# Kernel tuning notes

Measured on AMD Instinct MI355X. Metric: run time of the kernel, lower is better.

## Reference

```python
import jax, jax.numpy as jnp
import numpy as np

B_, L_, D_, N_ = 4, 4096, 1024, 32


def setup_inputs() -> dict:
    key = jax.random.key(0)
    ks = jax.random.split(key, 8)
    def n(k, shape, s=0.02):
        return jax.random.normal(k, shape, jnp.float32) * s
    return {
        "x": jax.random.normal(ks[0], (B_, L_, D_), jnp.float32),
        "in_w": n(ks[1], (2 * D_, D_)),
        "in_b": jnp.zeros((2 * D_,), jnp.float32),
        "conv_w": n(ks[2], (D_, 1, 4), 0.1),
        "conv_b": jnp.zeros((D_,), jnp.float32),
        "A_log": -2.0 + 0.1 * jax.random.normal(ks[3], (D_, N_), jnp.float32),
        "B_w": n(ks[4], (N_, D_)),
        "B_b": jnp.zeros((N_,), jnp.float32),
        "C_w": n(ks[5], (N_, D_)),
        "C_b": jnp.zeros((N_,), jnp.float32),
        "out_w": n(ks[6], (D_, D_)),
        "out_b": jnp.zeros((D_,), jnp.float32),
        "ln_w": jnp.ones((D_,), jnp.float32),
        "ln_b": jnp.zeros((D_,), jnp.float32),
    }


def reference(x, in_w, in_b, conv_w, conv_b, A_log, B_w, B_b, C_w, C_b, out_w, out_b, ln_w, ln_b):
    Bsz, L, D = x.shape
    residual = x
    # in_proj and chunk
    xz = x @ in_w.T + in_b                       # (B, L, 2D)
    xa, z = xz[..., :D], xz[..., D:]
    # depthwise conv1d, kernel=4, padding=2 -> length L+1 (matches torch)
    xc = jax.lax.conv_general_dilated(
        xa.transpose(0, 2, 1), conv_w, (1,), [(2, 2)],
        feature_group_count=D, dimension_numbers=("NCH", "OIH", "NCH"))
    xc = xc + conv_b[None, :, None]
    xc = jax.nn.silu(xc.transpose(0, 2, 1))      # (B, L+1, D)
    A = -jnp.exp(jnp.clip(A_log, -5.0, 2.0))     # (D, N)
    Bm = xc @ B_w.T + B_b                        # (B, L+1, N)
    Cm = xc @ C_w.T + C_b                        # (B, L+1, N)
    # only first L steps are used by the loop
    xs = (xc[:, :L].transpose(1, 0, 2),          # (L, B, D)
          Bm[:, :L].transpose(1, 0, 2),          # (L, B, N)
          Cm[:, :L].transpose(1, 0, 2))          # (L, B, N)
    s0 = jnp.zeros((Bsz, D, A.shape[1]), x.dtype)

    def step(s, t):
        x_t, b_t, c_t = t
        s = jnp.clip(s * A + b_t[:, None, :] * x_t[:, :, None], -10.0, 10.0)
        y = jnp.sum(c_t[:, None, :] * s, axis=-1)  # (B, D)
        return s, y

    _, ys = jax.lax.scan(step, s0, xs)           # ys: (L, B, D)
    y = ys.transpose(1, 0, 2) * jax.nn.silu(z)   # (B, L, D)
    out = y @ out_w.T + out_b
    h = out + residual
    mu = jnp.mean(h, axis=-1, keepdims=True)
    var = jnp.var(h, axis=-1, keepdims=True)
    return (h - mu) / jnp.sqrt(var + 1e-5) * ln_w + ln_b
```

## Files before the change

kernel.cpp:

```cpp
#include <hip/hip_runtime.h>
#include <hip/hip_bf16.h>

#define B_ 4
#define L_ 4096
#define D_ 1024
#define N_ 32
#define MTOT (B_*L_)
#define TCH 32
#define WARM 6
#define STEPS (TCH + WARM)
#define SROWS 48

typedef __bf16 bf16;
typedef __attribute__((ext_vector_type(8))) __bf16 bf16x8;
typedef __attribute__((ext_vector_type(4))) __bf16 bf16x4;
typedef __attribute__((ext_vector_type(4))) float f32x4;
typedef __attribute__((ext_vector_type(2))) float f32x2;

__device__ __forceinline__ void gload_lds16(const void* gsrc, void* ldst) {
  __builtin_amdgcn_global_load_lds(
      (__attribute__((address_space(1))) void*)(unsigned long long)gsrc,
      (__attribute__((address_space(3))) void*)ldst, 16, 0, 0);
}

__global__ __launch_bounds__(256) void cvt_w_kernel(
    const float* __restrict__ in_w, const float* __restrict__ out_w,
    const float* __restrict__ B_w, const float* __restrict__ C_w,
    const float* __restrict__ A_log, const float* __restrict__ B_b,
    const float* __restrict__ C_b, const float* __restrict__ x,
    bf16* __restrict__ in_wb, bf16* __restrict__ out_wb, bf16* __restrict__ bcw,
    float* __restrict__ Aexp, float* __restrict__ bias_bc,
    bf16* __restrict__ xb) {
  const int stride = gridDim.x * 256;
  const int i0 = blockIdx.x * 256 + threadIdx.x;
  for (int j = i0; j < (B_ * L_ * D_) / 4; j += stride) {
    const float4 v = ((const float4*)x)[j];
    bf16x4 o = {(bf16)v.x, (bf16)v.y, (bf16)v.z, (bf16)v.w};
    ((bf16x4*)xb)[j] = o;
  }
  for (int j = i0; j < 2 * D_ * D_; j += stride) in_wb[j] = (bf16)in_w[j];
  for (int j = i0; j < D_ * D_; j += stride) out_wb[j] = (bf16)out_w[j];
  for (int j = i0; j < N_ * D_; j += stride) {
    bcw[j] = (bf16)B_w[j];
    bcw[N_ * D_ + j] = (bf16)C_w[j];
  }
  for (int j = i0; j < D_ * N_; j += stride)
    Aexp[j] = -expf(fminf(fmaxf(A_log[j], -5.f), 2.f));
  if (i0 < N_) { bias_bc[i0] = B_b[i0]; bias_bc[N_ + i0] = C_b[i0]; }
}

template <bool OUT_BF16, bool ADD_RESID>
__global__ __launch_bounds__(256) void gemm8_kernel(
    const bf16* __restrict__ Ag, const bf16* __restrict__ Wg,
    const float* __restrict__ bias, const float* __restrict__ resid,
    void* __restrict__ Cg, int Ncols, int K, int nbm, int nbn) {
  constexpr int BK = 64;
  __shared__ bf16 As[2][128][64];
  __shared__ bf16 Bs[2][128][64];
  const int tid = threadIdx.x;
  const int lane = tid & 63;
  const int wid = tid >> 6;
  const int wm = wid >> 1, wn = wid & 1;
  const int l15 = lane & 15, lh = lane >> 4, r7 = l15 & 7;

  const int sx = nbm >> 3;
  const int xcd = blockIdx.x & 7;
  const int pos = blockIdx.x >> 3;
  const int bx = xcd * sx + pos / nbn;
  const int by = pos % nbn;
  const int row0 = bx * 128, col0 = by * 128;
  const int nt = K / BK;

  const bf16* aSrc[4]; const bf16* bSrc[4]; int dstOff[4];
#pragma unroll
  for (int j = 0; j < 4; ++j) {
    const int c = tid + j * 256;
    const int row = c >> 3, lcol = c & 7;
    const int gcol = lcol ^ (row & 7);
    aSrc[j] = Ag + (size_t)(row0 + row) * K + gcol * 8;
    bSrc[j] = Wg + (size_t)(col0 + row) * K + gcol * 8;
    dstOff[j] = c * 8;
  }

  f32x4 acc[4][4] = {};

#pragma unroll
  for (int j = 0; j < 4; ++j) gload_lds16(aSrc[j], &As[0][0][0] + dstOff[j]);
#pragma unroll
  for (int j = 0; j < 4; ++j) gload_lds16(bSrc[j], &Bs[0][0][0] + dstOff[j]);
#pragma unroll
  for (int j = 0; j < 4; ++j) gload_lds16(aSrc[j] + BK, &As[1][0][0] + dstOff[j]);
#pragma unroll
  for (int j = 0; j < 4; ++j) gload_lds16(bSrc[j] + BK, &Bs[1][0][0] + dstOff[j]);
  asm volatile("s_waitcnt vmcnt(8)" ::: "memory");
  __builtin_amdgcn_sched_barrier(0);
  __builtin_amdgcn_s_barrier();
  __builtin_amdgcn_sched_barrier(0);

  for (int t = 0; t < nt; ++t) {
    const int p = t & 1;
    const bf16* Ab = &As[p][0][0];
    const bf16* Bb = &Bs[p][0][0];
    bf16x8 af[4][2], bfr[4][2];
#pragma unroll
    for (int mi = 0; mi < 4; ++mi)
#pragma unroll
      for (int kk = 0; kk < 2; ++kk)
        af[mi][kk] = *(const bf16x8*)(Ab + (wm * 64 + mi * 16 + l15) * 64 +
                                      (((kk * 4 + lh) ^ r7) * 8));
#pragma unroll
    for (int ni = 0; ni < 4; ++ni)
#pragma unroll
      for (int kk = 0; kk < 2; ++kk)
        bfr[ni][kk] = *(const bf16x8*)(Bb + (wn * 64 + ni * 16 + l15) * 64 +
                                       (((kk * 4 + lh) ^ r7) * 8));
    asm volatile("s_waitcnt lgkmcnt(0)" ::: "memory");
    __builtin_amdgcn_sched_barrier(0);
    __builtin_amdgcn_s_barrier();
    __builtin_amdgcn_sched_barrier(0);
    if (t + 2 < nt) {
      const int k2 = (t + 2) * BK;
#pragma unroll
      for (int j = 0; j < 4; ++j) gload_lds16(aSrc[j] + k2, &As[p][0][0] + dstOff[j]);
#pragma unroll
      for (int j = 0; j < 4; ++j) gload_lds16(bSrc[j] + k2, &Bs[p][0][0] + dstOff[j]);
    }
    __builtin_amdgcn_s_setprio(1);
#pragma unroll
    for (int kk = 0; kk < 2; ++kk)
#pragma unroll
      for (int mi = 0; mi < 4; ++mi)
#pragma unroll
        for (int ni = 0; ni < 4; ++ni)
          acc[mi][ni] = __builtin_amdgcn_mfma_f32_16x16x32_bf16(
              af[mi][kk], bfr[ni][kk], acc[mi][ni], 0, 0, 0);
    __builtin_amdgcn_s_setprio(0);
    if (t + 2 < nt) asm volatile("s_waitcnt vmcnt(8)" ::: "memory");
    else            asm volatile("s_waitcnt vmcnt(0)" ::: "memory");
    __builtin_amdgcn_sched_barrier(0);
    __builtin_amdgcn_s_barrier();
    __builtin_amdgcn_sched_barrier(0);
  }

#pragma unroll
  for (int mi = 0; mi < 4; ++mi) {
#pragma unroll
    for (int ni = 0; ni < 4; ++ni) {
      const int c = col0 + wn * 64 + ni * 16 + l15;
      const float bv = bias[c];
#pragma unroll
      for (int j = 0; j < 4; ++j) {
        const int r = row0 + wm * 64 + mi * 16 + lh * 4 + j;
        float v = acc[mi][ni][j] + bv;
        if constexpr (ADD_RESID) v += resid[(size_t)r * Ncols + c];
        if constexpr (OUT_BF16)
          ((bf16*)Cg)[(size_t)r * Ncols + c] = (bf16)v;
        else
          ((float*)Cg)[(size_t)r * Ncols + c] = v;
      }
    }
  }
}

template <int BM, int BN, int WAVES_M, int WAVES_N, bool OUT_BF16, bool ADD_RESID>
__global__ __launch_bounds__(256) void gemm_kernel(
    const bf16* __restrict__ Ag, const bf16* __restrict__ Wg,
    const float* __restrict__ bias, const float* __restrict__ resid,
    void* __restrict__ Cg, int Ncols, int K) {
  constexpr int BK = 32;
  constexpr int WM = BM / WAVES_M;
  constexpr int WN = BN / WAVES_N;
  constexpr int MI = WM / 16;
  constexpr int NI = WN / 16;
  __shared__ alignas(16) bf16 As[BM][BK];
  __shared__ alignas(16) bf16 Bs[BN][BK];
  const int tid = threadIdx.x;
  const int lane = tid & 63;
  const int wid = tid >> 6;
  const int wm = wid / WAVES_N;
  const int wn = wid % WAVES_N;
  const int l15 = lane & 15;
  const int lh = lane >> 4;
  const int row0 = blockIdx.x * BM;
  const int col0 = blockIdx.y * BN;

  f32x4 acc[MI][NI] = {};

  for (int k0 = 0; k0 < K; k0 += BK) {
#pragma unroll
    for (int i = 0; i < (BM * BK * 2 / 16) / 256; ++i) {
      const int chunk = tid + i * 256;
      const int o = chunk * 16;
      const int r = o >> 6;
      const int kb = (o & 63) >> 1;
      gload_lds16(Ag + (size_t)(row0 + r) * K + (k0 + kb),
                  (bf16*)&As[0][0] + (size_t)(wid * 64 + i * 256) * 8);
    }
#pragma unroll
    for (int i = 0; i < (BN * BK * 2 / 16) / 256; ++i) {
      const int chunk = tid + i * 256;
      const int o = chunk * 16;
      const int r = o >> 6;
      const int kb = (o & 63) >> 1;
      gload_lds16(Wg + (size_t)(col0 + r) * K + (k0 + kb),
                  (bf16*)&Bs[0][0] + (size_t)(wid * 64 + i * 256) * 8);
    }
    __syncthreads();

    bf16x8 af[MI], bfv[NI];
#pragma unroll
    for (int mi = 0; mi < MI; ++mi)
      af[mi] = *(const bf16x8*)&As[wm * WM + mi * 16 + l15][lh * 8];
#pragma unroll
    for (int ni = 0; ni < NI; ++ni)
      bfv[ni] = *(const bf16x8*)&Bs[wn * WN + ni * 16 + l15][lh * 8];
#pragma unroll
    for (int mi = 0; mi < MI; ++mi)
#pragma unroll
      for (int ni = 0; ni < NI; ++ni)
        acc[mi][ni] = __builtin_amdgcn_mfma_f32_16x16x32_bf16(
            af[mi], bfv[ni], acc[mi][ni], 0, 0, 0);
    __syncthreads();
  }

#pragma unroll
  for (int mi = 0; mi < MI; ++mi) {
#pragma unroll
    for (int ni = 0; ni < NI; ++ni) {
      const int c = col0 + wn * WN + ni * 16 + l15;
      const float bv = bias[c];
#pragma unroll
      for (int j = 0; j < 4; ++j) {
        const int r = row0 + wm * WM + mi * 16 + lh * 4 + j;
        float v = acc[mi][ni][j] + bv;
        if constexpr (ADD_RESID) v += resid[(size_t)r * Ncols + c];
        if constexpr (OUT_BF16)
          ((bf16*)Cg)[(size_t)r * Ncols + c] = (bf16)v;
        else
          ((float*)Cg)[(size_t)r * Ncols + c] = v;
      }
    }
  }
}

__global__ __launch_bounds__(256) void conv_silu_kernel(
    const bf16* __restrict__ xz, const float* __restrict__ conv_w,
    const float* __restrict__ conv_b, bf16* __restrict__ xc) {
  const int idx = blockIdx.x * 256 + threadIdx.x;
  const int d8 = idx & (D_ / 8 - 1);
  const int bt = idx >> 7;
  const int t = bt & (L_ - 1);
  const int b = bt >> 12;
  const int d = d8 * 8;

  float accv[8];
  float4 w4[8];
#pragma unroll
  for (int j = 0; j < 8; ++j) {
    accv[j] = conv_b[d + j];
    w4[j] = *(const float4*)(conv_w + (size_t)(d + j) * 4);
  }
#pragma unroll
  for (int k = 0; k < 4; ++k) {
    const int tt = t + k - 2;
    if (tt < 0 || tt >= L_) continue;
    const bf16x8 xv = *(const bf16x8*)(xz + (size_t)(b * L_ + tt) * (2 * D_) + d);
#pragma unroll
    for (int j = 0; j < 8; ++j) {
      const float wk = (k == 0) ? w4[j].x : (k == 1) ? w4[j].y : (k == 2) ? w4[j].z : w4[j].w;
      accv[j] += (float)xv[j] * wk;
    }
  }
  bf16x8 o;
#pragma unroll
  for (int j = 0; j < 8; ++j) {
    const float v = accv[j];
    o[j] = (bf16)(v / (1.f + __expf(-v)));
  }
  *(bf16x8*)(xc + (size_t)(b * L_ + t) * D_ + d) = o;
}

#define SCAN_STEP(PB, PC, XT)                                             \
  {                                                                       \
    const f32x2 xt2 = {XT, XT};                                           \
    yac = (f32x2){0.f, 0.f};                                              \
    _Pragma("unroll")                                                     \
    for (int q = 0; q < 8; ++q) {                                         \
      f32x2 v = __builtin_elementwise_fma(s[q], Ar[q], PB[q] * xt2);      \
      s[q] = v;                                                           \
      yac = __builtin_elementwise_fma(PC[q], v, yac);                     \
    }                                                                     \
  }

__device__ __forceinline__ void load8v(f32x2* dst, const float* p) {
#pragma unroll
  for (int q = 0; q < 4; ++q) {
    const f32x4 v = ((const f32x4*)p)[q];
    dst[2 * q]     = (f32x2){v.x, v.y};
    dst[2 * q + 1] = (f32x2){v.z, v.w};
  }
}

__global__ __launch_bounds__(256)
__attribute__((amdgpu_waves_per_eu(4)))
void scan_kernel(
    const bf16* __restrict__ xc, const float* __restrict__ BC,
    const bf16* __restrict__ xz, const float* __restrict__ Aexp,
    bf16* __restrict__ y) {
  const int dg = blockIdx.x, chunk = blockIdx.y, b = blockIdx.z;
  const int tid = threadIdx.x;
  const int wid = tid >> 6;
  const int nh = tid & 1;
  const int dl = tid >> 1;
  const int d = dg * 128 + dl;
  const int t0 = chunk * TCH;
  const int warm = (t0 >= WARM) ? WARM : 0;
  const int tstart = t0 - warm;

  __shared__ float bcs[SROWS][64];
  __shared__ bf16 xcs[SROWS][128];
  __shared__ bf16 zs[TCH][128];

#pragma unroll
  for (int i = 0; i < 3; ++i)
    gload_lds16(BC + ((size_t)b * L_ + tstart) * 64 + (size_t)(tid + i * 256) * 4,
                (float*)&bcs[0][0] + (size_t)(wid * 64 + i * 256) * 4);
#pragma unroll
  for (int i = 0; i < 3; ++i) {
    const int c = tid + i * 256;
    gload_lds16(xc + ((size_t)b * L_ + tstart + (c >> 4)) * D_ + dg * 128 + (c & 15) * 8,
                (bf16*)&xcs[0][0] + (size_t)(wid * 64 + i * 256) * 8);
  }
#pragma unroll
  for (int i = 0; i < 2; ++i) {
    const int c = tid + i * 256;
    gload_lds16(xz + ((size_t)b * L_ + t0 + (c >> 4)) * (2 * D_) + D_ + dg * 128 + (c & 15) * 8,
                (bf16*)&zs[0][0] + (size_t)(wid * 64 + i * 256) * 8);
  }

  f32x2 Ar[8], s[8];
  {
    const f32x2* ap = (const f32x2*)(Aexp + (size_t)d * N_ + nh * 16);
#pragma unroll
    for (int q = 0; q < 8; ++q) { Ar[q] = ap[q]; s[q] = (f32x2){0.f, 0.f}; }
  }

  bf16* yp = y + (size_t)b * L_ * D_ + d;
  f32x2 yac;

  __syncthreads();

  for (int i = 0; i < warm; ++i) {
    const float xt = (float)xcs[i][dl];
    const f32x2 xt2 = {xt, xt};
    const f32x2* rb = (const f32x2*)&bcs[i][nh * 16];
#pragma unroll
    for (int q = 0; q < 8; ++q)
      s[q] = __builtin_elementwise_fma(s[q], Ar[q], rb[q] * xt2);
  }

  f32x2 pbA[8], pcA[8], pbB[8], pcB[8];
  float pxA, pzA, pxB, pzB;
  load8v(pbA, &bcs[warm][nh * 16]);
  load8v(pcA, &bcs[warm][32 + nh * 16]);
  pxA = (float)xcs[warm][dl];
  pzA = (float)zs[0][dl];

  for (int j = 0; j < TCH; j += 2) {
    load8v(pbB, &bcs[warm + j + 1][nh * 16]);
    load8v(pcB, &bcs[warm + j + 1][32 + nh * 16]);
    pxB = (float)xcs[warm + j + 1][dl];
    pzB = (float)zs[j + 1][dl];
    SCAN_STEP(pbA, pcA, pxA);
    {
      float yacc = yac.x + yac.y;
      yacc += __shfl_xor(yacc, 1);
      if (nh == 0) {
        const float sz = pzA / (1.f + __expf(-pzA));
        yp[(size_t)(t0 + j) * D_] = (bf16)(yacc * sz);
      }
    }
    load8v(pbA, &bcs[warm + j + 2][nh * 16]);
    load8v(pcA, &bcs[warm + j + 2][32 + nh * 16]);
    pxA = (float)xcs[warm + j + 2][dl];
    pzA = (float)zs[(j + 2 < TCH) ? (j + 2) : 0][dl];
    SCAN_STEP(pbB, pcB, pxB);
    {
      float yacc = yac.x + yac.y;
      yacc += __shfl_xor(yacc, 1);
      if (nh == 0) {
        const float sz = pzB / (1.f + __expf(-pzB));
        yp[(size_t)(t0 + j + 1) * D_] = (bf16)(yacc * sz);
      }
    }
  }
}

__global__ __launch_bounds__(256) void ln2_kernel(const bf16* __restrict__ g,
                                                  const float* __restrict__ x,
                                                  const float* __restrict__ ln_w,
                                                  const float* __restrict__ ln_b,
                                                  float* __restrict__ out) {
  const int row = blockIdx.x;
  const int tid = threadIdx.x;
  const bf16x4 gv = ((const bf16x4*)(g + (size_t)row * D_))[tid];
  const float4 xv = ((const float4*)(x + (size_t)row * D_))[tid];
  float4 v;
  v.x = (float)gv[0] + xv.x;
  v.y = (float)gv[1] + xv.y;
  v.z = (float)gv[2] + xv.z;
  v.w = (float)gv[3] + xv.w;
  float sum = v.x + v.y + v.z + v.w;
  float sq = v.x * v.x + v.y * v.y + v.z * v.z + v.w * v.w;
#pragma unroll
  for (int off = 32; off >= 1; off >>= 1) {
    sum += __shfl_xor(sum, off);
    sq += __shfl_xor(sq, off);
  }
  __shared__ float red[8];
  const int wid = tid >> 6;
  if ((tid & 63) == 0) { red[wid] = sum; red[4 + wid] = sq; }
  __syncthreads();
  sum = red[0] + red[1] + red[2] + red[3];
  sq = red[4] + red[5] + red[6] + red[7];
  const float mu = sum * (1.f / D_);
  const float var = sq * (1.f / D_) - mu * mu;
  const float inv = rsqrtf(var + 1e-5f);
  const float4 w4 = ((const float4*)ln_w)[tid];
  const float4 b4 = ((const float4*)ln_b)[tid];
  float4 o;
  o.x = (v.x - mu) * inv * w4.x + b4.x;
  o.y = (v.y - mu) * inv * w4.y + b4.y;
  o.z = (v.z - mu) * inv * w4.z + b4.z;
  o.w = (v.w - mu) * inv * w4.w + b4.w;
  ((float4*)(out + (size_t)row * D_))[tid] = o;
}

extern "C" void kernel_launch(void* const* d_in, const int* in_sizes, int n_in,
                              void* d_out, int out_size, void* d_ws, size_t ws_size,
                              hipStream_t stream) {
  (void)in_sizes; (void)n_in; (void)out_size; (void)ws_size;
  const float* x      = (const float*)d_in[0];
  const float* in_w   = (const float*)d_in[1];
  const float* in_b   = (const float*)d_in[2];
  const float* conv_w = (const float*)d_in[3];
  const float* conv_b = (const float*)d_in[4];
  const float* A_log  = (const float*)d_in[5];
  const float* B_w    = (const float*)d_in[6];
  const float* B_b    = (const float*)d_in[7];
  const float* C_w    = (const float*)d_in[8];
  const float* C_b    = (const float*)d_in[9];
  const float* out_w  = (const float*)d_in[10];
  const float* out_b  = (const float*)d_in[11];
  const float* ln_w   = (const float*)d_in[12];
  const float* ln_b   = (const float*)d_in[13];
  float* out = (float*)d_out;

  char* ws = (char*)d_ws;
  bf16* xb_y    = (bf16*)(ws + 0);
  bf16* xz      = (bf16*)(ws + 33554432);
  bf16* xc_g    = (bf16*)(ws + 100663296);
  float* BC     = (float*)(ws + 134217728);
  bf16* in_wb   = (bf16*)(ws + 138412032);
  bf16* out_wb  = (bf16*)(ws + 142606336);
  bf16* bcw     = (bf16*)(ws + 144703488);
  float* Aexp   = (float*)(ws + 144834560);
  float* bias_bc= (float*)(ws + 144965632);

  cvt_w_kernel<<<2048, 256, 0, stream>>>(in_w, out_w, B_w, C_w, A_log, B_b, C_b,
                                         x, in_wb, out_wb, bcw, Aexp, bias_bc, xb_y);
  gemm8_kernel<true, false>
      <<<128 * 16, 256, 0, stream>>>(xb_y, in_wb, in_b, nullptr, xz, 2 * D_, D_, 128, 16);
  conv_silu_kernel<<<(B_ * L_ * D_ / 8) / 256, 256, 0, stream>>>(xz, conv_w, conv_b, xc_g);
  gemm_kernel<64, 64, 2, 2, false, false>
      <<<dim3(MTOT / 64, 1), 256, 0, stream>>>(xc_g, bcw, bias_bc, nullptr, BC, 64, D_);
  scan_kernel<<<dim3(D_ / 128, L_ / TCH, B_), 256, 0, stream>>>(xc_g, BC, xz, Aexp, xb_y);
  gemm8_kernel<true, false>
      <<<128 * 8, 256, 0, stream>>>(xb_y, out_wb, out_b, nullptr, xc_g, D_, D_, 128, 8);
  ln2_kernel<<<MTOT, 256, 0, stream>>>(xc_g, x, ln_w, ln_b, out);
}
```

Measured before the change: 297.8 us.

## Replace 128x128 GEMM with 256x256-tile 8-wave kernel with interleaved staging

Replaces the 128x128-tile, 4-wave bf16 GEMM used for the in_proj and out_proj matmuls with a 256x256-tile, 512-thread kernel. Each wave computes a 128x64 sub-tile in four quarter phases, and global-to-LDS loads for the next K-steps are interleaved between the MFMA phases. Larger tiles raise arithmetic intensity and cut global traffic per FLOP. In exchange, the grid shrinks to 512 and 256 blocks, which can leave CUs underfilled on the out_proj launch, and the extra barriers per K-step add sync cost.

New measurement: 295.2 us. No clear change (-0.9%).

```diff
diff --git a/kernel.cpp b/kernel.cpp
--- a/kernel.cpp
+++ b/kernel.cpp
@@ -22,6 +22,11 @@
       (__attribute__((address_space(1))) void*)(unsigned long long)gsrc,
       (__attribute__((address_space(3))) void*)ldst, 16, 0, 0);
 }
+
+#define BARR  do { __builtin_amdgcn_s_barrier(); \
+                   __builtin_amdgcn_sched_barrier(0); } while (0)
+#define LGKM0 do { asm volatile("s_waitcnt lgkmcnt(0)" ::: "memory"); \
+                   __builtin_amdgcn_sched_barrier(0); } while (0)
 
 __global__ __launch_bounds__(256) void cvt_w_kernel(
     const float* __restrict__ in_w, const float* __restrict__ out_w,
@@ -49,114 +54,162 @@
   if (i0 < N_) { bias_bc[i0] = B_b[i0]; bias_bc[N_ + i0] = C_b[i0]; }
 }
 
-template <bool OUT_BF16, bool ADD_RESID>
-__global__ __launch_bounds__(256) void gemm8_kernel(
+__global__ __launch_bounds__(512, 1) void gemm256_kernel(
     const bf16* __restrict__ Ag, const bf16* __restrict__ Wg,
-    const float* __restrict__ bias, const float* __restrict__ resid,
-    void* __restrict__ Cg, int Ncols, int K, int nbm, int nbn) {
-  constexpr int BK = 64;
-  __shared__ bf16 As[2][128][64];
-  __shared__ bf16 Bs[2][128][64];
+    const float* __restrict__ bias, bf16* __restrict__ Cg,
+    int Ncols, int K, int nbm, int nbn) {
+  __shared__ bf16 lds[8][128][64];
   const int tid = threadIdx.x;
   const int lane = tid & 63;
   const int wid = tid >> 6;
-  const int wm = wid >> 1, wn = wid & 1;
-  const int l15 = lane & 15, lh = lane >> 4, r7 = l15 & 7;
+  const int wm = wid >> 2;
+  const int wn = wid & 3;
+  const int l15 = lane & 15, lh = lane >> 4;
 
   const int sx = nbm >> 3;
   const int xcd = blockIdx.x & 7;
   const int pos = blockIdx.x >> 3;
   const int bx = xcd * sx + pos / nbn;
   const int by = pos % nbn;
-  const int row0 = bx * 128, col0 = by * 128;
-  const int nt = K / BK;
-
-  const bf16* aSrc[4]; const bf16* bSrc[4]; int dstOff[4];
-#pragma unroll
-  for (int j = 0; j < 4; ++j) {
-    const int c = tid + j * 256;
-    const int row = c >> 3, lcol = c & 7;
-    const int gcol = lcol ^ (row & 7);
-    aSrc[j] = Ag + (size_t)(row0 + row) * K + gcol * 8;
-    bSrc[j] = Wg + (size_t)(col0 + row) * K + gcol * 8;
-    dstOff[j] = c * 8;
-  }
-
-  f32x4 acc[4][4] = {};
-
-#pragma unroll
-  for (int j = 0; j < 4; ++j) gload_lds16(aSrc[j], &As[0][0][0] + dstOff[j]);
-#pragma unroll
-  for (int j = 0; j < 4; ++j) gload_lds16(bSrc[j], &Bs[0][0][0] + dstOff[j]);
-#pragma unroll
-  for (int j = 0; j < 4; ++j) gload_lds16(aSrc[j] + BK, &As[1][0][0] + dstOff[j]);
-#pragma unroll
-  for (int j = 0; j < 4; ++j) gload_lds16(bSrc[j] + BK, &Bs[1][0][0] + dstOff[j]);
-  asm volatile("s_waitcnt vmcnt(8)" ::: "memory");
+  const int row0 = bx * 256, col0 = by * 256;
+  const int nt = K / 64;
+
+  const bf16* aS0; const bf16* aS1; const bf16* bS0; const bf16* bS1;
+  int dO0, dO1;
+  {
+    const int c0 = tid, c1 = tid + 512;
+    const int r0 = c0 >> 3, r1 = c1 >> 3;
+    const int g0 = (c0 & 7) ^ (r0 & 7), g1 = (c1 & 7) ^ (r1 & 7);
+    aS0 = Ag + (size_t)(row0 + r0) * K + g0 * 8;
+    aS1 = Ag + (size_t)(row0 + r1) * K + g1 * 8;
+    bS0 = Wg + (size_t)(col0 + r0) * K + g0 * 8;
+    bS1 = Wg + (size_t)(col0 + r1) * K + g1 * 8;
+    dO0 = c0 * 8; dO1 = c1 * 8;
+  }
+
+#define STAGE_A(T, HALF) do {                                               \
+    const size_t off_ = (size_t)(HALF) * 128 * K + (size_t)(T) * 64;        \
+    bf16* dst_ = &lds[((T) & 1) * 4 + (HALF)][0][0];                        \
+    gload_lds16(aS0 + off_, dst_ + dO0);                                    \
+    gload_lds16(aS1 + off_, dst_ + dO1); } while (0)
+#define STAGE_B(T, HALF) do {                                               \
+    const size_t off_ = (size_t)(HALF) * 128 * K + (size_t)(T) * 64;        \
+    bf16* dst_ = &lds[((T) & 1) * 4 + 2 + (HALF)][0][0];                    \
+    gload_lds16(bS0 + off_, dst_ + dO0);                                    \
+    gload_lds16(bS1 + off_, dst_ + dO1); } while (0)
+
+  f32x4 acc[8][4] = {};
+
+  STAGE_A(0, 0); STAGE_A(0, 1); STAGE_B(0, 0); STAGE_B(0, 1);
+  STAGE_B(1, 0); STAGE_B(1, 1);
+  asm volatile("s_waitcnt vmcnt(4)" ::: "memory");
   __builtin_amdgcn_sched_barrier(0);
-  __builtin_amdgcn_s_barrier();
-  __builtin_amdgcn_sched_barrier(0);
-
-  for (int t = 0; t < nt; ++t) {
-    const int p = t & 1;
-    const bf16* Ab = &As[p][0][0];
-    const bf16* Bb = &Bs[p][0][0];
-    bf16x8 af[4][2], bfr[4][2];
-#pragma unroll
-    for (int mi = 0; mi < 4; ++mi)
-#pragma unroll
-      for (int kk = 0; kk < 2; ++kk)
-        af[mi][kk] = *(const bf16x8*)(Ab + (wm * 64 + mi * 16 + l15) * 64 +
-                                      (((kk * 4 + lh) ^ r7) * 8));
-#pragma unroll
-    for (int ni = 0; ni < 4; ++ni)
-#pragma unroll
-      for (int kk = 0; kk < 2; ++kk)
-        bfr[ni][kk] = *(const bf16x8*)(Bb + (wn * 64 + ni * 16 + l15) * 64 +
-                                       (((kk * 4 + lh) ^ r7) * 8));
-    asm volatile("s_waitcnt lgkmcnt(0)" ::: "memory");
+  BARR;
+
+  for (int T = 0; T < nt; ++T) {
+    const int p = T & 1;
+    const bf16* Aseg = &lds[p * 4 + wm][0][0];
+    const bf16* Bseg = &lds[p * 4 + 2 + (wn >> 1)][0][0];
+    const int brow0 = (wn & 1) * 64;
+    bf16x8 af[4][2], bfv[4][2];
+    const bool s1 = (T + 1 < nt), s2 = (T + 2 < nt);
+
+    if (s1) STAGE_A(T + 1, 0);
+#pragma unroll
+    for (int mi = 0; mi < 4; ++mi) {
+      const int r = mi * 16 + l15, sw = r & 7;
+      af[mi][0] = *(const bf16x8*)(Aseg + r * 64 + ((lh ^ sw)) * 8);
+      af[mi][1] = *(const bf16x8*)(Aseg + r * 64 + (((4 + lh) ^ sw)) * 8);
+    }
+#pragma unroll
+    for (int ni = 0; ni < 2; ++ni) {
+      const int r = brow0 + ni * 16 + l15, sw = r & 7;
+      bfv[ni][0] = *(const bf16x8*)(Bseg + r * 64 + ((lh ^ sw)) * 8);
+      bfv[ni][1] = *(const bf16x8*)(Bseg + r * 64 + (((4 + lh) ^ sw)) * 8);
+    }
+    BARR; LGKM0;
+    __builtin_amdgcn_s_setprio(1);
+#pragma unroll
+    for (int kk = 0; kk < 2; ++kk)
+#pragma unroll
+      for (int mi = 0; mi < 4; ++mi)
+#pragma unroll
+        for (int ni = 0; ni < 2; ++ni)
+          acc[mi][ni] = __builtin_amdgcn_mfma_f32_16x16x32_bf16(
+              af[mi][kk], bfv[ni][kk], acc[mi][ni], 0, 0, 0);
+    __builtin_amdgcn_s_setprio(0);
+    BARR;
+
+    if (s1) STAGE_A(T + 1, 1);
+#pragma unroll
+    for (int ni = 2; ni < 4; ++ni) {
+      const int r = brow0 + ni * 16 + l15, sw = r & 7;
+      bfv[ni][0] = *(const bf16x8*)(Bseg + r * 64 + ((lh ^ sw)) * 8);
+      bfv[ni][1] = *(const bf16x8*)(Bseg + r * 64 + (((4 + lh) ^ sw)) * 8);
+    }
+    BARR; LGKM0;
+    __builtin_amdgcn_s_setprio(1);
+#pragma unroll
+    for (int kk = 0; kk < 2; ++kk)
+#pragma unroll
+      for (int mi = 0; mi < 4; ++mi)
+#pragma unroll
+        for (int ni = 2; ni < 4; ++ni)
+          acc[mi][ni] = __builtin_amdgcn_mfma_f32_16x16x32_bf16(
+              af[mi][kk], bfv[ni][kk], acc[mi][ni], 0, 0, 0);
+    __builtin_amdgcn_s_setprio(0);
+    BARR;
+
+    if (s2) STAGE_B(T + 2, 0);
+#pragma unroll
+    for (int mi = 0; mi < 4; ++mi) {
+      const int r = (mi + 4) * 16 + l15, sw = r & 7;
+      af[mi][0] = *(const bf16x8*)(Aseg + r * 64 + ((lh ^ sw)) * 8);
+      af[mi][1] = *(const bf16x8*)(Aseg + r * 64 + (((4 + lh) ^ sw)) * 8);
+    }
+    BARR; LGKM0;
+    __builtin_amdgcn_s_setprio(1);
+#pragma unroll
+    for (int kk = 0; kk < 2; ++kk)
+#pragma unroll
+      for (int mi = 0; mi < 4; ++mi)
+#pragma unroll
+        for (int ni = 0; ni < 2; ++ni)
+          acc[mi + 4][ni] = __builtin_amdgcn_mfma_f32_16x16x32_bf16(
+              af[mi][kk], bfv[ni][kk], acc[mi + 4][ni], 0, 0, 0);
+    __builtin_amdgcn_s_setprio(0);
+    BARR;
+
+    if (s2) STAGE_B(T + 2, 1);
+    BARR;
+    __builtin_amdgcn_s_setprio(1);
+#pragma unroll
+    for (int kk = 0; kk < 2; ++kk)
+#pragma unroll
+      for (int mi = 0; mi < 4; ++mi)
+#pragma unroll
+        for (int ni = 2; ni < 4; ++ni)
+          acc[mi + 4][ni] = __builtin_amdgcn_mfma_f32_16x16x32_bf16(
+              af[mi][kk], bfv[ni][kk], acc[mi + 4][ni], 0, 0, 0);
+    __builtin_amdgcn_s_setprio(0);
+    if (s2) asm volatile("s_waitcnt vmcnt(4)" ::: "memory");
+    else    asm volatile("s_waitcnt vmcnt(0)" ::: "memory");
     __builtin_amdgcn_sched_barrier(0);
-    __builtin_amdgcn_s_barrier();
-    __builtin_amdgcn_sched_barrier(0);
-    if (t + 2 < nt) {
-      const int k2 = (t + 2) * BK;
-#pragma unroll
-      for (int j = 0; j < 4; ++j) gload_lds16(aSrc[j] + k2, &As[p][0][0] + dstOff[j]);
-#pragma unroll
-      for (int j = 0; j < 4; ++j) gload_lds16(bSrc[j] + k2, &Bs[p][0][0] + dstOff[j]);
-    }
-    __builtin_amdgcn_s_setprio(1);
-#pragma unroll
-    for (int kk = 0; kk < 2; ++kk)
-#pragma unroll
-      for (int mi = 0; mi < 4; ++mi)
-#pragma unroll
-        for (int ni = 0; ni < 4; ++ni)
-          acc[mi][ni] = __builtin_amdgcn_mfma_f32_16x16x32_bf16(
-              af[mi][kk], bfr[ni][kk], acc[mi][ni], 0, 0, 0);
-    __builtin_amdgcn_s_setprio(0);
-    if (t + 2 < nt) asm volatile("s_waitcnt vmcnt(8)" ::: "memory");
-    else            asm volatile("s_waitcnt vmcnt(0)" ::: "memory");
-    __builtin_amdgcn_sched_barrier(0);
-    __builtin_amdgcn_s_barrier();
-    __builtin_amdgcn_sched_barrier(0);
-  }
-
-#pragma unroll
-  for (int mi = 0; mi < 4; ++mi) {
+    BARR;
+  }
+#undef STAGE_A
+#undef STAGE_B
+
+#pragma unroll
+  for (int mi = 0; mi < 8; ++mi) {
 #pragma unroll
     for (int ni = 0; ni < 4; ++ni) {
       const int c = col0 + wn * 64 + ni * 16 + l15;
       const float bv = bias[c];
 #pragma unroll
       for (int j = 0; j < 4; ++j) {
-        const int r = row0 + wm * 64 + mi * 16 + lh * 4 + j;
-        float v = acc[mi][ni][j] + bv;
-        if constexpr (ADD_RESID) v += resid[(size_t)r * Ncols + c];
-        if constexpr (OUT_BF16)
-          ((bf16*)Cg)[(size_t)r * Ncols + c] = (bf16)v;
-        else
-          ((float*)Cg)[(size_t)r * Ncols + c] = v;
+        const int r = row0 + wm * 128 + mi * 16 + lh * 4 + j;
+        Cg[(size_t)r * Ncols + c] = (bf16)(acc[mi][ni][j] + bv);
       }
     }
   }
@@ -469,13 +522,13 @@
 
   cvt_w_kernel<<<2048, 256, 0, stream>>>(in_w, out_w, B_w, C_w, A_log, B_b, C_b,
                                          x, in_wb, out_wb, bcw, Aexp, bias_bc, xb_y);
-  gemm8_kernel<true, false>
-      <<<128 * 16, 256, 0, stream>>>(xb_y, in_wb, in_b, nullptr, xz, 2 * D_, D_, 128, 16);
+  gemm256_kernel<<<64 * 8, 512, 0, stream>>>(xb_y, in_wb, in_b, xz,
+                                             2 * D_, D_, 64, 8);
   conv_silu_kernel<<<(B_ * L_ * D_ / 8) / 256, 256, 0, stream>>>(xz, conv_w, conv_b, xc_g);
   gemm_kernel<64, 64, 2, 2, false, false>
       <<<dim3(MTOT / 64, 1), 256, 0, stream>>>(xc_g, bcw, bias_bc, nullptr, BC, 64, D_);
   scan_kernel<<<dim3(D_ / 128, L_ / TCH, B_), 256, 0, stream>>>(xc_g, BC, xz, Aexp, xb_y);
-  gemm8_kernel<true, false>
-      <<<128 * 8, 256, 0, stream>>>(xb_y, out_wb, out_b, nullptr, xc_g, D_, D_, 128, 8);
+  gemm256_kernel<<<64 * 4, 512, 0, stream>>>(xb_y, out_wb, out_b, xc_g,
+                                             D_, D_, 64, 4);
   ln2_kernel<<<MTOT, 256, 0, stream>>>(xc_g, x, ln_w, ln_b, out);
 }
```
